# Kernel optimization log

Measured on AMD Instinct MI355X. Metric: run time of the kernel, lower is better.

## Reference

```python
import jax, jax.numpy as jnp
import numpy as np

N_NODES = 16384
N_EDGES = 65536
N_GRAPHS = 64


def setup_inputs() -> dict:
    key = jax.random.key(0)
    ks = iter(jax.random.split(key, 64))
    nk = lambda: next(ks)
    p = lambda *s: jax.random.normal(nk(), s, jnp.float32) * 0.1
    inp = {}
    inp['x'] = jax.random.normal(nk(), (N_NODES, 1), jnp.float32)
    inp['edge_index'] = jax.random.randint(nk(), (2, N_EDGES), 0, N_NODES, dtype=jnp.int32)
    inp['batch'] = jnp.sort(jax.random.randint(nk(), (N_NODES,), 0, N_GRAPHS, dtype=jnp.int32))
    for i, (fi, fo) in [(1, (1, 64)), (2, (64, 512)), (3, (512, 2048))]:
        inp[f'gat{i}_wl'] = p(fi, fo)
        inp[f'gat{i}_wr'] = p(fi, fo)
        inp[f'gat{i}_att'] = p(fo)
        inp[f'gat{i}_b'] = jnp.zeros((fo,), jnp.float32)
    for i, c in [(1, 64), (2, 512), (3, 2048), (4, 512), (5, 64)]:
        inp[f'gn{i}_w'] = jnp.ones((c,), jnp.float32)
        inp[f'gn{i}_b'] = jnp.zeros((c,), jnp.float32)
        inp[f'gn{i}_ms'] = jnp.ones((c,), jnp.float32)
    for i, (fi, fo) in [(1, (2048, 512)), (2, (512, 64))]:
        inp[f'arma{i}_wi'] = p(fi, fo)
        inp[f'arma{i}_wr'] = p(fi, fo)
        inp[f'arma{i}_b'] = jnp.zeros((fo,), jnp.float32)
    inp['lin_w'] = p(192, 2)
    inp['lin_b'] = jnp.zeros((2,), jnp.float32)
    return inp


def _seg_softmax(e, idx, n):
    m = jax.ops.segment_max(e, idx, num_segments=n)
    ex = jnp.exp(e - m[idx])
    s = jax.ops.segment_sum(ex, idx, num_segments=n)
    return ex / (s[idx] + 1e-16)


def _gatv2(x, src, dst, wl, wr, att, b):
    # GATv2: e_ij = a^T LeakyReLU(W_l x_j + W_r x_i), softmax over dst neighborhoods
    n = x.shape[0]
    xl = x @ wl
    xr = x @ wr
    e = jax.nn.leaky_relu(xl[src] + xr[dst], 0.2) @ att  # [E]
    a = _seg_softmax(e, dst, n)
    return jax.ops.segment_sum(xl[src] * a[:, None], dst, num_segments=n) + b


def _graph_norm(x, batch, w, b, ms, cnt):
    mean = jax.ops.segment_sum(x, batch, num_segments=N_GRAPHS) / cnt
    out = x - mean[batch] * ms
    var = jax.ops.segment_sum(out * out, batch, num_segments=N_GRAPHS) / cnt
    return w * out / jnp.sqrt(var + 1e-5)[batch] + b


def _arma(x, src, dst, norm, wi, wr, b):
    # ARMAConv, num_stacks=1, num_layers=1: ReLU(Ahat (x Wi) + x Wr + b)
    agg = jax.ops.segment_sum((x @ wi)[src] * norm[:, None], dst, num_segments=x.shape[0])
    return jax.nn.relu(agg + x @ wr + b)


def _forward(x, edge_index, batch,
             gat1_wl, gat1_wr, gat1_att, gat1_b, gn1_w, gn1_b, gn1_ms,
             gat2_wl, gat2_wr, gat2_att, gat2_b, gn2_w, gn2_b, gn2_ms,
             gat3_wl, gat3_wr, gat3_att, gat3_b, gn3_w, gn3_b, gn3_ms,
             arma1_wi, arma1_wr, arma1_b, gn4_w, gn4_b, gn4_ms,
             arma2_wi, arma2_wr, arma2_b, gn5_w, gn5_b, gn5_ms,
             lin_w, lin_b):
    n = x.shape[0]
    src, dst = edge_index[0], edge_index[1]
    sl = jnp.arange(n, dtype=edge_index.dtype)
    src_sl = jnp.concatenate([src, sl])  # GATv2 adds self loops
    dst_sl = jnp.concatenate([dst, sl])
    # gcn_norm without self loops (ARMAConv default)
    deg = jax.ops.segment_sum(jnp.ones_like(src, dtype=x.dtype), dst, num_segments=n)
    dis = jnp.where(deg > 0, 1.0 / jnp.sqrt(jnp.maximum(deg, 1.0)), 0.0)
    norm = dis[src] * dis[dst]
    cnt = jnp.maximum(jax.ops.segment_sum(jnp.ones((n,), x.dtype), batch, num_segments=N_GRAPHS), 1.0)[:, None]

    h = jax.nn.elu(_gatv2(x, src_sl, dst_sl, gat1_wl, gat1_wr, gat1_att, gat1_b))
    h = _graph_norm(h, batch, gn1_w, gn1_b, gn1_ms, cnt)
    h = jax.nn.elu(_gatv2(h, src_sl, dst_sl, gat2_wl, gat2_wr, gat2_att, gat2_b))
    h = _graph_norm(h, batch, gn2_w, gn2_b, gn2_ms, cnt)
    h = jax.nn.elu(_gatv2(h, src_sl, dst_sl, gat3_wl, gat3_wr, gat3_att, gat3_b))
    h = _graph_norm(h, batch, gn3_w, gn3_b, gn3_ms, cnt)
    h = jax.nn.elu(_arma(h, src, dst, norm, arma1_wi, arma1_wr, arma1_b))
    h = _graph_norm(h, batch, gn4_w, gn4_b, gn4_ms, cnt)
    h = jax.nn.elu(_arma(h, src, dst, norm, arma2_wi, arma2_wr, arma2_b))
    h = _graph_norm(h, batch, gn5_w, gn5_b, gn5_ms, cnt)

    x_max = jax.ops.segment_max(h, batch, num_segments=N_GRAPHS)
    x_sum = jax.ops.segment_sum(h, batch, num_segments=N_GRAPHS)
    x_mean = x_sum / cnt
    return jnp.concatenate([x_max, x_mean, x_sum], axis=1) @ lin_w + lin_b


def reference(x, edge_index, batch,
              gat1_wl, gat1_wr, gat1_att, gat1_b, gn1_w, gn1_b, gn1_ms,
              gat2_wl, gat2_wr, gat2_att, gat2_b, gn2_w, gn2_b, gn2_ms,
              gat3_wl, gat3_wr, gat3_att, gat3_b, gn3_w, gn3_b, gn3_ms,
              arma1_wi, arma1_wr, arma1_b, gn4_w, gn4_b, gn4_ms,
              arma2_wi, arma2_wr, arma2_b, gn5_w, gn5_b, gn5_ms,
              lin_w, lin_b):
    return _forward(x, edge_index, batch,
                    gat1_wl, gat1_wr, gat1_att, gat1_b, gn1_w, gn1_b, gn1_ms,
                    gat2_wl, gat2_wr, gat2_att, gat2_b, gn2_w, gn2_b, gn2_ms,
                    gat3_wl, gat3_wr, gat3_att, gat3_b, gn3_w, gn3_b, gn3_ms,
                    arma1_wi, arma1_wr, arma1_b, gn4_w, gn4_b, gn4_ms,
                    arma2_wi, arma2_wr, arma2_b, gn5_w, gn5_b, gn5_ms,
                    lin_w, lin_b)
```

## Files before the change

kernel.cpp:

```cpp
#include <hip/hip_runtime.h>
#include <hip/hip_bf16.h>

#define NN 16384
#define NE 65536
#define NESL (NE + NN)
#define NG 64

typedef __hip_bfloat16 bf16;
typedef __attribute__((ext_vector_type(8))) short short8v;
typedef __attribute__((ext_vector_type(4))) short short4v;
typedef __attribute__((ext_vector_type(4))) float f32x4;
typedef __attribute__((address_space(3))) void lds_void;
typedef const __attribute__((address_space(1))) void glb_void;

__device__ __forceinline__ short bfbits(float v) {
  bf16 h = __float2bfloat16(v);
  return *(short*)&h;
}
__device__ __forceinline__ float bfs2f(short s) {
  return __uint_as_float(((unsigned)(unsigned short)s) << 16);
}
__device__ __forceinline__ void gld16(const void* g, void* l) {
  __builtin_amdgcn_global_load_lds((glb_void*)g, (lds_void*)l, 16, 0, 0);
}

__global__ void k_zero2(int* a, int* b, int n) {
  int i = blockIdx.x * blockDim.x + threadIdx.x;
  if (i < n) { a[i] = 0; b[i] = 0; }
}


__global__ void k_ranges(const int* __restrict__ batch, int* __restrict__ R,
                         float* __restrict__ cnt) {
  int g = threadIdx.x;
  if (g <= NG) {
    int lo = 0, hi = NN;
    while (lo < hi) { int mid = (lo + hi) >> 1; if (batch[mid] < g) lo = mid + 1; else hi = mid; }
    R[g] = lo;
  }
  __syncthreads();
  if (g < NG) cnt[g] = fmaxf((float)(R[g + 1] - R[g]), 1.0f);
}

__global__ void k_deg(const int* __restrict__ dst, int* __restrict__ deg) {
  int e = blockIdx.x * blockDim.x + threadIdx.x;
  if (e < NE) atomicAdd(deg + dst[e], 1);
}

__global__ void k_dis(const int* __restrict__ deg, float* __restrict__ dis) {
  int n = blockIdx.x * blockDim.x + threadIdx.x;
  if (n < NN) { int d = deg[n]; dis[n] = d > 0 ? 1.0f / sqrtf((float)d) : 0.0f; }
}

__global__ void k_scan(const int* __restrict__ deg, int* __restrict__ rowptr) {
  __shared__ int sums[1024];
  int tid = threadIdx.x;
  int base = tid * 16;
  int loc[16];
  int run = 0;
#pragma unroll
  for (int i = 0; i < 16; i++) { run += deg[base + i] + 1; loc[i] = run; }
  sums[tid] = run;
  __syncthreads();
  for (int off = 1; off < 1024; off <<= 1) {
    int v = sums[tid];
    int u = (tid >= off) ? sums[tid - off] : 0;
    __syncthreads();
    sums[tid] = v + u;
    __syncthreads();
  }
  int offset = (tid > 0) ? sums[tid - 1] : 0;
  if (tid == 0) rowptr[0] = 0;
#pragma unroll
  for (int i = 0; i < 16; i++) rowptr[base + i + 1] = loc[i] + offset;
}

__global__ void k_fill(const int* __restrict__ src, const int* __restrict__ dst,
                       const int* __restrict__ rowptr, const float* __restrict__ dis,
                       int* __restrict__ fill, int* __restrict__ srck,
                       float* __restrict__ normk) {
  int e = blockIdx.x * blockDim.x + threadIdx.x;
  if (e >= NESL) return;
  int s = e < NE ? src[e] : e - NE;
  int d = e < NE ? dst[e] : e - NE;
  int pos = rowptr[d] + atomicAdd(fill + d, 1);
  srck[pos] = s;
  normk[pos] = e < NE ? dis[s] * dis[d] : 0.0f;
}

__device__ __forceinline__ size_t pidx(int n, int k, int K) {
  size_t t = (size_t)(n >> 7) * (K >> 5) + (k >> 5);
  int col = n & 127, kk = k & 31;
  int lane = ((kk >> 3) << 4) | (col & 15);
  return t * 4096 + (size_t)((col >> 4) * 512 + lane * 8 + (kk & 7));
}

__global__ void k_wsplit_pk(const float* __restrict__ w, short* __restrict__ hi,
                            short* __restrict__ lo, int K, int N, int n0) {
  int i = blockIdx.x * blockDim.x + threadIdx.x;
  if (i >= N * K) return;
  int n = i / K, k = i % K;
  float v = w[(size_t)k * N + n];
  short h = bfbits(v);
  size_t pi = pidx(n0 + n, k, K);
  hi[pi] = h;
  lo[pi] = bfbits(v - bfs2f(h));
}

template <int SPLITA, int CBF16, int ACT>
__global__ __launch_bounds__(256) void gemm_mfma_p(const short* __restrict__ Ahi,
                                                   const short* __restrict__ Alo,
                                                   const short* __restrict__ Bthi,
                                                   const short* __restrict__ Btlo,
                                                   void* __restrict__ Cp,
                                                   const float* __restrict__ bias,
                                                   int M, int N, int K) {
  __shared__ __align__(16) short sA[2][(SPLITA ? 2 : 1) * 4096];
  __shared__ __align__(16) short sB[2][8192];
  const int tid = threadIdx.x;
  const int wave = tid >> 6, lane = tid & 63;
  const int wm = wave >> 1, wn = wave & 1;
  const int row0 = blockIdx.y * 128, col0 = blockIdx.x * 128;
  const int nkb = K >> 5;
  const int c = wave * 2;
  const int ar = lane & 15, akc = lane >> 4;
  f32x4 acc[4][4] = {};

  auto stage = [&](int buf, int kb) {
    const short* bh = Bthi + ((size_t)(col0 >> 7) * nkb + kb) * 4096;
    const short* bl = Btlo + ((size_t)(col0 >> 7) * nkb + kb) * 4096;
    gld16(bh + (size_t)c * 512 + lane * 8, (char*)sB[buf] + c * 1024);
    gld16(bh + (size_t)(c + 1) * 512 + lane * 8, (char*)sB[buf] + (c + 1) * 1024);
    gld16(bl + (size_t)c * 512 + lane * 8, (char*)sB[buf] + 8192 + c * 1024);
    gld16(bl + (size_t)(c + 1) * 512 + lane * 8, (char*)sB[buf] + 8192 + (c + 1) * 1024);
    gld16(Ahi + (size_t)(row0 + c * 16 + ar) * K + kb * 32 + akc * 8,
          (char*)sA[buf] + c * 1024);
    gld16(Ahi + (size_t)(row0 + (c + 1) * 16 + ar) * K + kb * 32 + akc * 8,
          (char*)sA[buf] + (c + 1) * 1024);
    if constexpr (SPLITA) {
      gld16(Alo + (size_t)(row0 + c * 16 + ar) * K + kb * 32 + akc * 8,
            (char*)sA[buf] + 8192 + c * 1024);
      gld16(Alo + (size_t)(row0 + (c + 1) * 16 + ar) * K + kb * 32 + akc * 8,
            (char*)sA[buf] + 8192 + (c + 1) * 1024);
    }
  };

  stage(0, 0);
  for (int kb = 0; kb < nkb; kb++) {
    int cur = kb & 1;
    if (kb + 1 < nkb) {
      stage(cur ^ 1, kb + 1);
      if constexpr (SPLITA)
        asm volatile("s_waitcnt vmcnt(8)" ::: "memory");
      else
        asm volatile("s_waitcnt vmcnt(6)" ::: "memory");
    } else {
      asm volatile("s_waitcnt vmcnt(0)" ::: "memory");
    }
    __builtin_amdgcn_sched_barrier(0);
    __builtin_amdgcn_s_barrier();
    __builtin_amdgcn_sched_barrier(0);
    asm volatile("" ::: "memory");
    short8v af[4], al[4], bh[4], bl[4];
#pragma unroll
    for (int f = 0; f < 4; f++) {
      af[f] = *(short8v*)((char*)sA[cur] + (wm * 4 + f) * 1024 + lane * 16);
      if constexpr (SPLITA)
        al[f] = *(short8v*)((char*)sA[cur] + 8192 + (wm * 4 + f) * 1024 + lane * 16);
      bh[f] = *(short8v*)((char*)sB[cur] + (wn * 4 + f) * 1024 + lane * 16);
      bl[f] = *(short8v*)((char*)sB[cur] + 8192 + (wn * 4 + f) * 1024 + lane * 16);
    }
#pragma unroll
    for (int i = 0; i < 4; i++)
#pragma unroll
      for (int j = 0; j < 4; j++) {
        acc[i][j] = __builtin_amdgcn_mfma_f32_16x16x32_bf16(af[i], bh[j], acc[i][j], 0, 0, 0);
        acc[i][j] = __builtin_amdgcn_mfma_f32_16x16x32_bf16(af[i], bl[j], acc[i][j], 0, 0, 0);
        if constexpr (SPLITA)
          acc[i][j] = __builtin_amdgcn_mfma_f32_16x16x32_bf16(al[i], bh[j], acc[i][j], 0, 0, 0);
      }
    asm volatile("" ::: "memory");
    __builtin_amdgcn_sched_barrier(0);
    __builtin_amdgcn_s_barrier();
    __builtin_amdgcn_sched_barrier(0);
  }
#pragma unroll
  for (int i = 0; i < 4; i++)
#pragma unroll
    for (int j = 0; j < 4; j++)
#pragma unroll
      for (int r = 0; r < 4; r++) {
        int row = row0 + wm * 64 + i * 16 + ((lane >> 4) << 2) + r;
        int col = col0 + wn * 64 + j * 16 + (lane & 15);
        float v = acc[i][j][r];
        if (bias) v += bias[col];
        if constexpr (ACT == 1) v = v > 0.0f ? v : expf(v) - 1.0f;
        if constexpr (ACT == 2) v = fmaxf(v, 0.0f);
        if constexpr (CBF16) {
          ((short*)Cp)[(size_t)row * N + col] = bfbits(v);
        } else {
          ((float*)Cp)[(size_t)row * N + col] = v;
        }
      }
}

__global__ void k_gat1_csr(const float* __restrict__ x, const float* __restrict__ wl,
                           const float* __restrict__ wr, const float* __restrict__ att,
                           const int* __restrict__ rowptr, const int* __restrict__ srck,
                           float* __restrict__ ework, const float* __restrict__ bias,
                           float* __restrict__ out) {
  int node = blockIdx.x * 4 + (threadIdx.x >> 6);
  int lane = threadIdx.x & 63;
  float wlv = wl[lane], wrv = wr[lane], av = att[lane];
  float xd = x[node];
  int beg = rowptr[node], end = rowptr[node + 1];
  float m = -INFINITY;
  for (int k = beg; k < end; k++) {
    float v = x[srck[k]] * wlv + xd * wrv;
    v = v > 0.0f ? v : 0.2f * v;
    float e = av * v;
#pragma unroll
    for (int off = 32; off; off >>= 1) e += __shfl_xor(e, off);
    if (lane == 0) ework[k] = e;
    m = fmaxf(m, e);
  }
  __syncthreads();
  float sum = 0.0f, agg = 0.0f;
  for (int k = beg + lane; k < end; k += 64) {
    float p = expf(ework[k] - m);
    sum += p;
    agg += p * x[srck[k]];
  }
#pragma unroll
  for (int off = 32; off; off >>= 1) {
    sum += __shfl_xor(sum, off);
    agg += __shfl_xor(agg, off);
  }
  float o = agg / (sum + 1e-16f) * wlv + bias[lane];
  out[(size_t)node * 64 + lane] = o > 0.0f ? o : expf(o) - 1.0f;
}

template <int FO, int STR, typename XT>
__global__ void k_logits_csr(const XT* __restrict__ X, const float* __restrict__ att,
                             const int* __restrict__ rowptr, const int* __restrict__ srck,
                             float* __restrict__ pk, float* __restrict__ ssum) {
  int node = blockIdx.x * 4 + (threadIdx.x >> 6);
  int lane = threadIdx.x & 63;
  constexpr int NV = FO / 64;
  float xr[NV], at[NV];
  if constexpr (sizeof(XT) == 2) {
    const short* xrp = (const short*)X + (size_t)node * STR + FO;
#pragma unroll
    for (int j = 0; j < FO / 512; j++) {
      short8v v = *(const short8v*)(xrp + j * 512 + lane * 8);
      f32x4 a0 = *(const f32x4*)(att + j * 512 + lane * 8);
      f32x4 a1 = *(const f32x4*)(att + j * 512 + lane * 8 + 4);
#pragma unroll
      for (int t = 0; t < 8; t++) {
        xr[j * 8 + t] = bfs2f(v[t]);
        at[j * 8 + t] = t < 4 ? a0[t] : a1[t - 4];
      }
    }
  } else {
    const float* xrp = (const float*)X + (size_t)node * STR + FO;
#pragma unroll
    for (int j = 0; j < FO / 256; j++) {
      f32x4 v = *(const f32x4*)(xrp + j * 256 + lane * 4);
      f32x4 a = *(const f32x4*)(att + j * 256 + lane * 4);
#pragma unroll
      for (int t = 0; t < 4; t++) {
        xr[j * 4 + t] = v[t];
        at[j * 4 + t] = a[t];
      }
    }
  }
  int beg = rowptr[node], end = rowptr[node + 1];
  float m = -INFINITY;
  for (int k = beg; k < end; k++) {
    int s = srck[k];
    float acc = 0.0f;
    if constexpr (sizeof(XT) == 2) {
      const short* xlp = (const short*)X + (size_t)s * STR;
#pragma unroll
      for (int j = 0; j < FO / 512; j++) {
        short8v v = *(const short8v*)(xlp + j * 512 + lane * 8);
#pragma unroll
        for (int t = 0; t < 8; t++) {
          float u = bfs2f(v[t]) + xr[j * 8 + t];
          u = u > 0.0f ? u : 0.2f * u;
          acc += at[j * 8 + t] * u;
        }
      }
    } else {
      const float* xlp = (const float*)X + (size_t)s * STR;
#pragma unroll
      for (int j = 0; j < FO / 256; j++) {
        f32x4 v = *(const f32x4*)(xlp + j * 256 + lane * 4);
#pragma unroll
        for (int t = 0; t < 4; t++) {
          float u = v[t] + xr[j * 4 + t];
          u = u > 0.0f ? u : 0.2f * u;
          acc += at[j * 4 + t] * u;
        }
      }
    }
#pragma unroll
    for (int off = 32; off; off >>= 1) acc += __shfl_xor(acc, off);
    if (lane == 0) pk[k] = acc;
    m = fmaxf(m, acc);
  }
  __syncthreads();
  float sum = 0.0f;
  for (int k = beg + lane; k < end; k += 64) {
    float p = expf(pk[k] - m);
    pk[k] = p;
    sum += p;
  }
#pragma unroll
  for (int off = 32; off; off >>= 1) sum += __shfl_xor(sum, off);
  if (lane == 0) ssum[node] = sum;
}

template <int MODE, int SSTR, int OSTR>
__global__ void k_agg512(const float* __restrict__ Xsrc, const float* __restrict__ pk,
                         const float* __restrict__ ssum, const int* __restrict__ rowptr,
                         const int* __restrict__ srck, const float* __restrict__ normk,
                         const float* __restrict__ xwrb, const float* __restrict__ bias,
                         float* __restrict__ out, short* __restrict__ outhi,
                         short* __restrict__ outlo) {
  int wave = threadIdx.x >> 6;
  int node = blockIdx.x * 2 + (wave >> 1);
  int lane = threadIdx.x & 63;
  int c0 = (wave & 1) * 256 + lane * 4;
  f32x4 acc = {};
  int beg = rowptr[node], end = rowptr[node + 1];
  float inv = (MODE == 0) ? 1.0f / (ssum[node] + 1e-16f) : 1.0f;
  for (int k = beg; k < end; k++) {
    int s = srck[k];
    float w = (MODE == 0) ? pk[k] * inv : normk[k];
    f32x4 v = *(const f32x4*)(Xsrc + (size_t)s * SSTR + c0);
#pragma unroll
    for (int t = 0; t < 4; t++) acc[t] += w * v[t];
  }
  if constexpr (MODE == 1) {
    f32x4 xv = *(const f32x4*)(xwrb + (size_t)node * SSTR + 512 + c0);
#pragma unroll
    for (int t = 0; t < 4; t++) acc[t] = fmaxf(acc[t] + xv[t] + bias[c0 + t], 0.0f);
    *(f32x4*)(out + (size_t)node * OSTR + c0) = acc;
  } else {
    short4v hh, ll;
#pragma unroll
    for (int t = 0; t < 4; t++) {
      hh[t] = bfbits(acc[t]);
      ll[t] = bfbits(acc[t] - bfs2f(hh[t]));
    }
    *(short4v*)(outhi + (size_t)node * OSTR + c0) = hh;
    *(short4v*)(outlo + (size_t)node * OSTR + c0) = ll;
  }
}

template <int MODE, int SSTR, int XOFF>
__global__ void k_agg64(const float* __restrict__ Xsrc, const float* __restrict__ pk,
                        const float* __restrict__ ssum, const int* __restrict__ rowptr,
                        const int* __restrict__ srck, const float* __restrict__ normk,
                        const float* __restrict__ xwrb, const float* __restrict__ bias,
                        float* __restrict__ out, short* __restrict__ outhi,
                        short* __restrict__ outlo) {
  int node = blockIdx.x * (blockDim.x >> 6) + (threadIdx.x >> 6);
  if (node >= NN) return;
  int lane = threadIdx.x & 63;
  int cg = lane & 15, eg = lane >> 4;
  int c0 = cg * 4;
  f32x4 acc = {};
  int beg = rowptr[node], end = rowptr[node + 1];
  float inv = (MODE == 0) ? 1.0f / (ssum[node] + 1e-16f) : 1.0f;
  for (int k = beg + eg; k < end; k += 4) {
    int s = srck[k];
    float w = (MODE == 0) ? pk[k] * inv : normk[k];
    f32x4 v = *(const f32x4*)(Xsrc + (size_t)s * SSTR + c0);
#pragma unroll
    for (int t = 0; t < 4; t++) acc[t] += w * v[t];
  }
#pragma unroll
  for (int t = 0; t < 4; t++) {
    acc[t] += __shfl_xor(acc[t], 16);
    acc[t] += __shfl_xor(acc[t], 32);
  }
  if (eg == 0) {
    if constexpr (MODE == 1) {
      f32x4 xv = *(const f32x4*)(xwrb + (size_t)node * SSTR + XOFF + c0);
#pragma unroll
      for (int t = 0; t < 4; t++) acc[t] = fmaxf(acc[t] + xv[t] + bias[c0 + t], 0.0f);
      *(f32x4*)(out + (size_t)node * 64 + c0) = acc;
    } else {
      short4v hh, ll;
#pragma unroll
      for (int t = 0; t < 4; t++) {
        hh[t] = bfbits(acc[t]);
        ll[t] = bfbits(acc[t] - bfs2f(hh[t]));
      }
      *(short4v*)(outhi + (size_t)node * 64 + c0) = hh;
      *(short4v*)(outlo + (size_t)node * 64 + c0) = ll;
    }
  }
}

template <typename T, int VEC>
__global__ void k_gn_stats_v(const T* __restrict__ x, const int* __restrict__ R, int C,
                             float* __restrict__ s1, float* __restrict__ s2) {
  int g = blockIdx.x;
  int c0 = (blockIdx.y * blockDim.x + threadIdx.x) * VEC;
  if (c0 >= C) return;
  int beg = R[g], end = R[g + 1];
  float a[VEC] = {}, b[VEC] = {};
  for (int n = beg; n < end; n++) {
    const T* p = x + (size_t)n * C + c0;
    float v[VEC];
    if constexpr (sizeof(T) == 2) {
      short8v h = *(const short8v*)p;
#pragma unroll
      for (int t = 0; t < VEC; t++) v[t] = bfs2f(h[t]);
    } else {
      f32x4 h = *(const f32x4*)p;
#pragma unroll
      for (int t = 0; t < VEC; t++) v[t] = h[t];
    }
#pragma unroll
    for (int t = 0; t < VEC; t++) {
      a[t] += v[t];
      b[t] += v[t] * v[t];
    }
  }
#pragma unroll
  for (int t = 0; t < VEC; t++) {
    s1[g * C + c0 + t] = a[t];
    s2[g * C + c0 + t] = b[t];
  }
}

template <typename T, int VEC, int EMIT>
__global__ void k_gn_apply_v(T* __restrict__ x, const int* __restrict__ batch,
                             const float* __restrict__ cnt, const float* __restrict__ s1,
                             const float* __restrict__ s2, const float* __restrict__ w,
                             const float* __restrict__ b, const float* __restrict__ ms, int C,
                             int total_vec, short* __restrict__ hip,
                             short* __restrict__ lop) {
  int i = blockIdx.x * blockDim.x + threadIdx.x;
  if (i >= total_vec) return;
  int cpv = C / VEC;
  int n = i / cpv, c0 = (i % cpv) * VEC;
  int g = batch[n];
  float ct = cnt[g];
  T* p = x + (size_t)n * C + c0;
  float v[VEC];
  if constexpr (sizeof(T) == 2) {
    short8v h = *(const short8v*)p;
#pragma unroll
    for (int t = 0; t < VEC; t++) v[t] = bfs2f(h[t]);
  } else {
    f32x4 h = *(const f32x4*)p;
#pragma unroll
    for (int t = 0; t < VEC; t++) v[t] = h[t];
  }
#pragma unroll
  for (int t = 0; t < VEC; t++) {
    int cc = c0 + t;
    float mean = s1[g * C + cc] / ct;
    float mm = mean * ms[cc];
    float var = s2[g * C + cc] / ct - 2.0f * mm * mean + mm * mm;
    v[t] = (v[t] - mm) * (1.0f / sqrtf(var + 1e-5f)) * w[cc] + b[cc];
  }
  if constexpr (sizeof(T) == 2) {
    short8v h;
#pragma unroll
    for (int t = 0; t < VEC; t++) h[t] = bfbits(v[t]);
    *(short8v*)p = h;
  } else {
    f32x4 h;
#pragma unroll
    for (int t = 0; t < VEC; t++) h[t] = v[t];
    *(f32x4*)p = h;
  }
  if constexpr (EMIT >= 2) {
    short4v hh;
#pragma unroll
    for (int t = 0; t < VEC; t++) hh[t] = bfbits(v[t]);
    *(short4v*)(hip + (size_t)n * C + c0) = hh;
    if constexpr (EMIT == 3) {
      short4v ll;
#pragma unroll
      for (int t = 0; t < VEC; t++) ll[t] = bfbits(v[t] - bfs2f(hh[t]));
      *(short4v*)(lop + (size_t)n * C + c0) = ll;
    }
  }
}

__global__ void k_pool(const float* __restrict__ h, const int* __restrict__ R,
                       const float* __restrict__ cnt, const float* __restrict__ lw,
                       const float* __restrict__ lb, float* __restrict__ out) {
  int g = blockIdx.x;
  int c = threadIdx.x;
  int beg = R[g], end = R[g + 1];
  float mx = -INFINITY, sm = 0.0f;
  for (int n = beg; n < end; n++) {
    float v = h[(size_t)n * 64 + c];
    mx = fmaxf(mx, v);
    sm += v;
  }
  __shared__ float feat[192];
  feat[c] = mx;
  feat[64 + c] = sm / cnt[g];
  feat[128 + c] = sm;
  __syncthreads();
  if (c < 2) {
    float acc = lb[c];
    for (int j = 0; j < 192; j++) acc += feat[j] * lw[j * 2 + c];
    out[g * 2 + c] = acc;
  }
}


extern "C" void kernel_launch(void* const* d_in, const int* in_sizes, int n_in,
                              void* d_out, int out_size, void* d_ws, size_t ws_size,
                              hipStream_t stream) {
  const float* x = (const float*)d_in[0];
  const int* ei = (const int*)d_in[1];
  const int* batch = (const int*)d_in[2];
  const float* g1wl = (const float*)d_in[3];
  const float* g1wr = (const float*)d_in[4];
  const float* g1att = (const float*)d_in[5];
  const float* g1b = (const float*)d_in[6];
  const float* g2wl = (const float*)d_in[7];
  const float* g2wr = (const float*)d_in[8];
  const float* g2att = (const float*)d_in[9];
  const float* g2b = (const float*)d_in[10];
  const float* g3wl = (const float*)d_in[11];
  const float* g3wr = (const float*)d_in[12];
  const float* g3att = (const float*)d_in[13];
  const float* g3b = (const float*)d_in[14];
  const float* gn1w = (const float*)d_in[15];
  const float* gn1b = (const float*)d_in[16];
  const float* gn1ms = (const float*)d_in[17];
  const float* gn2w = (const float*)d_in[18];
  const float* gn2b = (const float*)d_in[19];
  const float* gn2ms = (const float*)d_in[20];
  const float* gn3w = (const float*)d_in[21];
  const float* gn3b = (const float*)d_in[22];
  const float* gn3ms = (const float*)d_in[23];
  const float* gn4w = (const float*)d_in[24];
  const float* gn4b = (const float*)d_in[25];
  const float* gn4ms = (const float*)d_in[26];
  const float* gn5w = (const float*)d_in[27];
  const float* gn5b = (const float*)d_in[28];
  const float* gn5ms = (const float*)d_in[29];
  const float* a1wi = (const float*)d_in[30];
  const float* a1wr = (const float*)d_in[31];
  const float* a1b = (const float*)d_in[32];
  const float* a2wi = (const float*)d_in[33];
  const float* a2wr = (const float*)d_in[34];
  const float* a2b = (const float*)d_in[35];
  const float* linw = (const float*)d_in[36];
  const float* linb = (const float*)d_in[37];
  const int* srcp = ei;
  const int* dstp = ei + NE;
  float* out = (float*)d_out;

  float* ws = (float*)d_ws;
  size_t o = 0;
  auto alloc = [&](size_t nfloats) { float* p = ws + o; o += nfloats; return p; };
  float* BIG0f = alloc((size_t)NN * 1024);
  float* BIG1f = alloc((size_t)NN * 1024);
  float* B0 = alloc((size_t)NN * 512);
  float* B1 = alloc((size_t)NN * 512);
  float* h1 = alloc((size_t)NN * 64);
  float* S0 = alloc((size_t)NN * 64);
  float* S1 = alloc((size_t)NN * 64);
  float* S2 = alloc((size_t)NN * 64);
  float* pk = alloc(NESL);
  float* normk = alloc(NESL);
  float* ssum = alloc(NN);
  float* dis = alloc(NN);
  float* cnt = alloc(NG);
  float* s1 = alloc(NG * 2048);
  float* s2 = alloc(NG * 2048);
  short* WThi = (short*)alloc((size_t)4096 * 512 / 2);
  short* WTlo = (short*)alloc((size_t)4096 * 512 / 2);
  int* deg = (int*)alloc(NN);
  int* rowptr = (int*)alloc(NN + 1);
  int* fill = (int*)alloc(NN);
  int* srck = (int*)alloc(NESL);
  int* R = (int*)alloc(72);

  bf16* XLR3 = (bf16*)BIG0f;
  bf16* h3 = (bf16*)BIG0f;
  float* h4 = BIG1f;
  short* h4hi = (short*)BIG0f;
  short* h4lo = h4hi + (size_t)NN * 512;
  float* XLR2 = B0;
  float* h2 = B0;
  short* h2hi = (short*)B1;
  short* agg2hi = (short*)B1;
  short* agg2lo = agg2hi + (size_t)NN * 512;
  float* TXW1 = B0;
  float* TXW2 = S0;
  short* h1hi = (short*)S2;
  short* h1lo = h1hi + (size_t)NN * 64;
  short* aggShi = (short*)S0;
  short* aggSlo = aggShi + (size_t)NN * 64;
  float* h5 = S2;

  k_zero2<<<NN / 256, 256, 0, stream>>>(deg, fill, NN);
  k_ranges<<<1, 128, 0, stream>>>(batch, R, cnt);
  k_deg<<<NE / 256, 256, 0, stream>>>(dstp, deg);
  k_scan<<<1, 1024, 0, stream>>>(deg, rowptr);
  k_dis<<<NN / 256, 256, 0, stream>>>(deg, dis);
  k_fill<<<(NESL + 255) / 256, 256, 0, stream>>>(srcp, dstp, rowptr, dis, fill, srck, normk);

  k_gat1_csr<<<NN / 4, 256, 0, stream>>>(x, g1wl, g1wr, g1att, rowptr, srck, pk, g1b, h1);
  k_gn_stats_v<float, 4><<<dim3(NG, 1), 16, 0, stream>>>(h1, R, 64, s1, s2);
  k_gn_apply_v<float, 4, 3><<<NN * 16 / 256, 256, 0, stream>>>(h1, batch, cnt, s1, s2, gn1w,
                                                               gn1b, gn1ms, 64, NN * 16, h1hi,
                                                               h1lo);

  k_wsplit_pk<<<(512 * 64 + 255) / 256, 256, 0, stream>>>(g2wl, WThi, WTlo, 64, 512, 0);
  k_wsplit_pk<<<(512 * 64 + 255) / 256, 256, 0, stream>>>(g2wr, WThi, WTlo, 64, 512, 512);
  gemm_mfma_p<1, 0, 0><<<dim3(8, 128), 256, 0, stream>>>(h1hi, h1lo, WThi, WTlo, XLR2, nullptr,
                                                         NN, 1024, 64);
  k_logits_csr<512, 1024, float><<<NN / 4, 256, 0, stream>>>(XLR2, g2att, rowptr, srck, pk, ssum);
  k_agg64<0, 64, 0><<<NN / 4, 256, 0, stream>>>(h1, pk, ssum, rowptr, srck, normk, nullptr,
                                                nullptr, nullptr, aggShi, aggSlo);
  gemm_mfma_p<1, 0, 1><<<dim3(4, 128), 256, 0, stream>>>(aggShi, aggSlo, WThi, WTlo, h2, g2b,
                                                         NN, 512, 64);
  k_gn_stats_v<float, 4><<<dim3(NG, 1), 128, 0, stream>>>(h2, R, 512, s1, s2);
  k_gn_apply_v<float, 4, 2><<<NN * 128 / 256, 256, 0, stream>>>(h2, batch, cnt, s1, s2, gn2w,
                                                                gn2b, gn2ms, 512, NN * 128,
                                                                h2hi, nullptr);

  k_wsplit_pk<<<(2048 * 512 + 255) / 256, 256, 0, stream>>>(g3wl, WThi, WTlo, 512, 2048, 0);
  k_wsplit_pk<<<(2048 * 512 + 255) / 256, 256, 0, stream>>>(g3wr, WThi, WTlo, 512, 2048, 2048);
  gemm_mfma_p<0, 1, 0><<<dim3(32, 128), 256, 0, stream>>>(h2hi, nullptr, WThi, WTlo, XLR3,
                                                          nullptr, NN, 4096, 512);
  k_logits_csr<2048, 4096, bf16><<<NN / 4, 256, 0, stream>>>(XLR3, g3att, rowptr, srck, pk, ssum);
  k_agg512<0, 512, 512><<<NN / 2, 256, 0, stream>>>(h2, pk, ssum, rowptr, srck, normk, nullptr,
                                                    nullptr, nullptr, agg2hi, agg2lo);
  gemm_mfma_p<1, 1, 1><<<dim3(16, 128), 256, 0, stream>>>(agg2hi, agg2lo, WThi, WTlo, h3, g3b,
                                                          NN, 2048, 512);
  k_gn_stats_v<bf16, 8><<<dim3(NG, 1), 256, 0, stream>>>(h3, R, 2048, s1, s2);
  k_gn_apply_v<bf16, 8, 0><<<NN * 256 / 256, 256, 0, stream>>>(h3, batch, cnt, s1, s2, gn3w,
                                                               gn3b, gn3ms, 2048, NN * 256,
                                                               nullptr, nullptr);

  k_wsplit_pk<<<(512 * 2048 + 255) / 256, 256, 0, stream>>>(a1wi, WThi, WTlo, 2048, 512, 0);
  k_wsplit_pk<<<(512 * 2048 + 255) / 256, 256, 0, stream>>>(a1wr, WThi, WTlo, 2048, 512, 512);
  gemm_mfma_p<0, 0, 0><<<dim3(8, 128), 256, 0, stream>>>((const short*)h3, nullptr, WThi, WTlo,
                                                         TXW1, nullptr, NN, 1024, 2048);
  k_agg512<1, 1024, 512><<<NN / 2, 256, 0, stream>>>(TXW1, pk, nullptr, rowptr, srck, normk,
                                                     TXW1, a1b, h4, nullptr, nullptr);
  k_gn_stats_v<float, 4><<<dim3(NG, 1), 128, 0, stream>>>(h4, R, 512, s1, s2);
  k_gn_apply_v<float, 4, 3><<<NN * 128 / 256, 256, 0, stream>>>(h4, batch, cnt, s1, s2, gn4w,
                                                                gn4b, gn4ms, 512, NN * 128,
                                                                h4hi, h4lo);

  k_wsplit_pk<<<(64 * 512 + 255) / 256, 256, 0, stream>>>(a2wi, WThi, WTlo, 512, 64, 0);
  k_wsplit_pk<<<(64 * 512 + 255) / 256, 256, 0, stream>>>(a2wr, WThi, WTlo, 512, 64, 64);
  gemm_mfma_p<1, 0, 0><<<dim3(1, 128), 256, 0, stream>>>(h4hi, h4lo, WThi, WTlo, TXW2, nullptr,
                                                         NN, 128, 512);
  k_agg64<1, 128, 64><<<NN / 4, 256, 0, stream>>>(TXW2, pk, nullptr, rowptr, srck, normk, TXW2,
                                                  a2b, h5, nullptr, nullptr);
  k_gn_stats_v<float, 4><<<dim3(NG, 1), 16, 0, stream>>>(h5, R, 64, s1, s2);
  k_gn_apply_v<float, 4, 0><<<NN * 16 / 256, 256, 0, stream>>>(h5, batch, cnt, s1, s2, gn5w,
                                                               gn5b, gn5ms, 64, NN * 16, nullptr,
                                                               nullptr);

  k_pool<<<NG, 64, 0, stream>>>(h5, R, cnt, linw, linb, out);
}
```

Baseline: 1.317 ms.

## Fuse weight split kernels, swizzle GEMM block order, store layer-2 projections as bf16

Each pair of weight hi/lo split-and-pack launches becomes one kernel, where each thread writes a contiguous 8-element packed group with vector stores instead of scattered 2-byte writes. The GEMM remaps its block index so that consecutive workgroups are spread across groups of eight, which changes which tiles run together and how they share cache. The layer-2 GATv2 projection output is now written in bf16 and the logits kernel reads bf16, halving that intermediate's traffic at some cost in precision for the attention logits.

```diff
diff --git a/kernel.cpp b/kernel.cpp
--- a/kernel.cpp
+++ b/kernel.cpp
@@ -88,23 +88,30 @@
   normk[pos] = e < NE ? dis[s] * dis[d] : 0.0f;
 }
 
-__device__ __forceinline__ size_t pidx(int n, int k, int K) {
-  size_t t = (size_t)(n >> 7) * (K >> 5) + (k >> 5);
-  int col = n & 127, kk = k & 31;
-  int lane = ((kk >> 3) << 4) | (col & 15);
-  return t * 4096 + (size_t)((col >> 4) * 512 + lane * 8 + (kk & 7));
-}
-
-__global__ void k_wsplit_pk(const float* __restrict__ w, short* __restrict__ hi,
-                            short* __restrict__ lo, int K, int N, int n0) {
-  int i = blockIdx.x * blockDim.x + threadIdx.x;
-  if (i >= N * K) return;
-  int n = i / K, k = i % K;
-  float v = w[(size_t)k * N + n];
-  short h = bfbits(v);
-  size_t pi = pidx(n0 + n, k, K);
-  hi[pi] = h;
-  lo[pi] = bfbits(v - bfs2f(h));
+__global__ void k_wsplit2(const float* __restrict__ wa, const float* __restrict__ wb,
+                          short* __restrict__ hi, short* __restrict__ lo, int K, int Nw) {
+  int gi = blockIdx.x * blockDim.x + threadIdx.x;
+  int ngroups = (Nw >> 6) * (K >> 5) * 512;
+  if (gi >= ngroups) return;
+  int g = gi & 511;
+  int t = gi >> 9;
+  int nkb = K >> 5;
+  int tn = t / nkb, tk = t % nkb;
+  int lane = g & 63;
+  int n = tn * 128 + ((g >> 6) << 4) + (lane & 15);
+  int kb = tk * 32 + ((lane >> 4) << 3);
+  const float* w = (n < Nw) ? wa : wb;
+  int nn = (n < Nw) ? n : n - Nw;
+  short8v h, l;
+#pragma unroll
+  for (int j = 0; j < 8; j++) {
+    float v = w[(size_t)(kb + j) * Nw + nn];
+    short hb = bfbits(v);
+    h[j] = hb;
+    l[j] = bfbits(v - bfs2f(hb));
+  }
+  *(short8v*)(hi + (size_t)gi * 8) = h;
+  *(short8v*)(lo + (size_t)gi * 8) = l;
 }
 
 template <int SPLITA, int CBF16, int ACT>
@@ -120,7 +127,11 @@
   const int tid = threadIdx.x;
   const int wave = tid >> 6, lane = tid & 63;
   const int wm = wave >> 1, wn = wave & 1;
-  const int row0 = blockIdx.y * 128, col0 = blockIdx.x * 128;
+  const int nbx = gridDim.x;
+  const int nwg = nbx * gridDim.y;
+  const int hw = blockIdx.y * nbx + blockIdx.x;
+  const int lg = (hw & 7) * (nwg >> 3) + (hw >> 3);
+  const int row0 = (lg / nbx) * 128, col0 = (lg % nbx) * 128;
   const int nkb = K >> 5;
   const int c = wave * 2;
   const int ar = lane & 15, akc = lane >> 4;
@@ -596,7 +607,7 @@
   float* h4 = BIG1f;
   short* h4hi = (short*)BIG0f;
   short* h4lo = h4hi + (size_t)NN * 512;
-  float* XLR2 = B0;
+  short* XLR2 = (short*)B0;
   float* h2 = B0;
   short* h2hi = (short*)B1;
   short* agg2hi = (short*)B1;
@@ -622,11 +633,11 @@
                                                                gn1b, gn1ms, 64, NN * 16, h1hi,
                                                                h1lo);
 
-  k_wsplit_pk<<<(512 * 64 + 255) / 256, 256, 0, stream>>>(g2wl, WThi, WTlo, 64, 512, 0);
-  k_wsplit_pk<<<(512 * 64 + 255) / 256, 256, 0, stream>>>(g2wr, WThi, WTlo, 64, 512, 512);
-  gemm_mfma_p<1, 0, 0><<<dim3(8, 128), 256, 0, stream>>>(h1hi, h1lo, WThi, WTlo, XLR2, nullptr,
+  k_wsplit2<<<8192 / 256, 256, 0, stream>>>(g2wl, g2wr, WThi, WTlo, 64, 512);
+  gemm_mfma_p<1, 1, 0><<<dim3(8, 128), 256, 0, stream>>>(h1hi, h1lo, WThi, WTlo, XLR2, nullptr,
                                                          NN, 1024, 64);
-  k_logits_csr<512, 1024, float><<<NN / 4, 256, 0, stream>>>(XLR2, g2att, rowptr, srck, pk, ssum);
+  k_logits_csr<512, 1024, bf16><<<NN / 4, 256, 0, stream>>>((const bf16*)XLR2, g2att, rowptr,
+                                                            srck, pk, ssum);
   k_agg64<0, 64, 0><<<NN / 4, 256, 0, stream>>>(h1, pk, ssum, rowptr, srck, normk, nullptr,
                                                 nullptr, nullptr, aggShi, aggSlo);
   gemm_mfma_p<1, 0, 1><<<dim3(4, 128), 256, 0, stream>>>(aggShi, aggSlo, WThi, WTlo, h2, g2b,
@@ -636,8 +647,7 @@
                                                                 gn2b, gn2ms, 512, NN * 128,
                                                                 h2hi, nullptr);
 
-  k_wsplit_pk<<<(2048 * 512 + 255) / 256, 256, 0, stream>>>(g3wl, WThi, WTlo, 512, 2048, 0);
-  k_wsplit_pk<<<(2048 * 512 + 255) / 256, 256, 0, stream>>>(g3wr, WThi, WTlo, 512, 2048, 2048);
+  k_wsplit2<<<262144 / 256, 256, 0, stream>>>(g3wl, g3wr, WThi, WTlo, 512, 2048);
   gemm_mfma_p<0, 1, 0><<<dim3(32, 128), 256, 0, stream>>>(h2hi, nullptr, WThi, WTlo, XLR3,
                                                           nullptr, NN, 4096, 512);
   k_logits_csr<2048, 4096, bf16><<<NN / 4, 256, 0, stream>>>(XLR3, g3att, rowptr, srck, pk, ssum);
@@ -650,8 +660,7 @@
                                                                gn3b, gn3ms, 2048, NN * 256,
                                                                nullptr, nullptr);
 
-  k_wsplit_pk<<<(512 * 2048 + 255) / 256, 256, 0, stream>>>(a1wi, WThi, WTlo, 2048, 512, 0);
-  k_wsplit_pk<<<(512 * 2048 + 255) / 256, 256, 0, stream>>>(a1wr, WThi, WTlo, 2048, 512, 512);
+  k_wsplit2<<<262144 / 256, 256, 0, stream>>>(a1wi, a1wr, WThi, WTlo, 2048, 512);
   gemm_mfma_p<0, 0, 0><<<dim3(8, 128), 256, 0, stream>>>((const short*)h3, nullptr, WThi, WTlo,
                                                          TXW1, nullptr, NN, 1024, 2048);
   k_agg512<1, 1024, 512><<<NN / 2, 256, 0, stream>>>(TXW1, pk, nullptr, rowptr, srck, normk,
@@ -661,8 +670,7 @@
                                                                 gn4b, gn4ms, 512, NN * 128,
                                                                 h4hi, h4lo);
 
-  k_wsplit_pk<<<(64 * 512 + 255) / 256, 256, 0, stream>>>(a2wi, WThi, WTlo, 512, 64, 0);
-  k_wsplit_pk<<<(64 * 512 + 255) / 256, 256, 0, stream>>>(a2wr, WThi, WTlo, 512, 64, 64);
+  k_wsplit2<<<8192 / 256, 256, 0, stream>>>(a2wi, a2wr, WThi, WTlo, 512, 64);
   gemm_mfma_p<1, 0, 0><<<dim3(1, 128), 256, 0, stream>>>(h4hi, h4lo, WThi, WTlo, TXW2, nullptr,
                                                          NN, 128, 512);
   k_agg64<1, 128, 64><<<NN / 4, 256, 0, stream>>>(TXW2, pk, nullptr, rowptr, srck, normk, TXW2,
```

Measured after the change: 1.279 ms. 2.9% less time.
